# Kernel optimization log

Hardware: AMD Instinct MI355X
Metric: run time of the kernel (lower is better)

## Reference

```python
import jax, jax.numpy as jnp
import numpy as np

N = 8192
H = 512

def setup_inputs() -> dict:
    key = jax.random.key(0)
    ks = jax.random.split(key, 11)
    s = 1.0 / np.sqrt(H)
    return {
        "q": jax.random.normal(ks[0], (N, H), dtype=jnp.float32),
        "k": jax.random.normal(ks[1], (N, H), dtype=jnp.float32),
        "v": jax.random.normal(ks[2], (N, H), dtype=jnp.float32),
        "Wq": jax.random.uniform(ks[3], (H, H), jnp.float32, -s, s),
        "bq": jax.random.uniform(ks[4], (H,), jnp.float32, -s, s),
        "Wk": jax.random.uniform(ks[5], (H, H), jnp.float32, -s, s),
        "bk": jax.random.uniform(ks[6], (H,), jnp.float32, -s, s),
        "Wv": jax.random.uniform(ks[7], (H, H), jnp.float32, -s, s),
        "bv": jax.random.uniform(ks[8], (H,), jnp.float32, -s, s),
        "Wo": jax.random.uniform(ks[9], (H, H), jnp.float32, -s, s),
        "bo": jax.random.uniform(ks[10], (H,), jnp.float32, -s, s),
    }

def reference(q, k, v, Wq, bq, Wk, bk, Wv, bv, Wo, bo):
    # torch Linear: x @ W.T + b
    qp = q @ Wq.T + bq            # [N, H]
    kp = k @ Wk.T + bk            # [N, H]
    vp = v @ Wv.T + bv            # [N, H]
    weights = qp @ kp.T           # [N, N]  (no 1/sqrt(d) scaling in original)
    normalized = jax.nn.softmax(weights, axis=-1)  # [N, N]
    out = normalized @ vp         # [N, H]
    out = out @ Wo.T + bo         # [N, H]
    return (out, normalized)
```

## Files before the change

### kernel.cpp

```cpp
#include <hip/hip_runtime.h>

typedef unsigned short u16;
typedef _Float16 f16x8 __attribute__((ext_vector_type(8)));
typedef u16 u16x8 __attribute__((ext_vector_type(8)));
typedef float floatx4 __attribute__((ext_vector_type(4)));

#define DEV __device__ __forceinline__

DEV u16 f2h(float f) {
  _Float16 h = (_Float16)f;
  return __builtin_bit_cast(u16, h);
}

typedef __attribute__((address_space(3))) void lds_void_t;
typedef const __attribute__((address_space(1))) void gbl_void_t;

DEV void async16(const void* g, void* l) {
  __builtin_amdgcn_global_load_lds((gbl_void_t*)g, (lds_void_t*)l, 16, 0, 0);
}

template <int N>
DEV void wait_vm() {
  static_assert(N == 0 || N == 6 || N == 8 || N == 9 || N == 12,
                "add vmcnt literal");
  if constexpr (N == 0) asm volatile("s_waitcnt vmcnt(0)" ::: "memory");
  else if constexpr (N == 6) asm volatile("s_waitcnt vmcnt(6)" ::: "memory");
  else if constexpr (N == 8) asm volatile("s_waitcnt vmcnt(8)" ::: "memory");
  else if constexpr (N == 9) asm volatile("s_waitcnt vmcnt(9)" ::: "memory");
  else if constexpr (N == 12) asm volatile("s_waitcnt vmcnt(12)" ::: "memory");
}


__global__ __launch_bounds__(256) void k_cvt16(const float* __restrict__ x,
                                               u16* __restrict__ o, int n4) {
  int i = blockIdx.x * 256 + threadIdx.x;
  if (i >= n4) return;
  float4 v = ((const float4*)x)[i];
  *(ushort4*)&o[4 * (size_t)i] =
      make_ushort4(f2h(v.x), f2h(v.y), f2h(v.z), f2h(v.w));
}


__global__ __launch_bounds__(256) void k_transpose(const u16* __restrict__ in,
                                                   u16* __restrict__ out,
                                                   int R, int C) {
  __shared__ u16 T[64][72];
  int m0 = blockIdx.x * 64;
  int n0 = blockIdx.y * 64;
  int t = threadIdx.x;
#pragma unroll
  for (int i = 0; i < 2; ++i) {
    int lin = i * 2048 + t * 8;
    int r = lin >> 6, c = lin & 63;
    u16x8 d = *(const u16x8*)&in[(size_t)(m0 + r) * C + n0 + c];
#pragma unroll
    for (int j = 0; j < 8; ++j) T[r][c + j] = d[j];
  }
  __syncthreads();
#pragma unroll
  for (int i = 0; i < 2; ++i) {
    int lin = i * 2048 + t * 8;
    int r = lin >> 6, c = lin & 63;
    u16x8 d;
#pragma unroll
    for (int j = 0; j < 8; ++j) d[j] = T[c + j][r];
    *(u16x8*)&out[(size_t)(n0 + r) * R + m0 + c] = d;
  }
}


template <bool WRITEP>
__global__ __launch_bounds__(256) void k_softmax(float* __restrict__ W,
                                                 u16* __restrict__ P) {
  const size_t row = blockIdx.x;
  float4* pv = (float4*)(W + row * 8192);
  const int t = threadIdx.x;
  const int w = t >> 6, l = t & 63;
  float4 v[8];
#pragma unroll
  for (int i = 0; i < 8; ++i) v[i] = pv[i * 256 + t];
  float m = -1e30f;
#pragma unroll
  for (int i = 0; i < 8; ++i)
    m = fmaxf(m, fmaxf(fmaxf(v[i].x, v[i].y), fmaxf(v[i].z, v[i].w)));
#pragma unroll
  for (int o = 32; o >= 1; o >>= 1) m = fmaxf(m, __shfl_xor(m, o, 64));
  __shared__ float redm[4];
  __shared__ float reds[4];
  if (l == 0) redm[w] = m;
  __syncthreads();
  m = fmaxf(fmaxf(redm[0], redm[1]), fmaxf(redm[2], redm[3]));
  float s = 0.f;
#pragma unroll
  for (int i = 0; i < 8; ++i) {
    v[i].x = __expf(v[i].x - m); s += v[i].x;
    v[i].y = __expf(v[i].y - m); s += v[i].y;
    v[i].z = __expf(v[i].z - m); s += v[i].z;
    v[i].w = __expf(v[i].w - m); s += v[i].w;
  }
#pragma unroll
  for (int o = 32; o >= 1; o >>= 1) s += __shfl_xor(s, o, 64);
  if (l == 0) reds[w] = s;
  __syncthreads();
  s = (reds[0] + reds[1]) + (reds[2] + reds[3]);
  float inv = 1.0f / s;
#pragma unroll
  for (int i = 0; i < 8; ++i) {
    v[i].x *= inv; v[i].y *= inv; v[i].z *= inv; v[i].w *= inv;
    pv[i * 256 + t] = v[i];
    if constexpr (WRITEP) {
      *(ushort4*)&P[row * 8192 + (size_t)(i * 256 + t) * 4] =
          make_ushort4(f2h(v[i].x), f2h(v[i].y), f2h(v[i].z), f2h(v[i].w));
    }
  }
}


template <int BN, bool AF32, int OMODE, bool BIAS>
__global__ __launch_bounds__(256, 2)
void k_gemm(const void* A_, const u16* __restrict__ Bh,
            const float* __restrict__ bias, void* C_, int K, int lda, int ldb,
            int ldc) {
  constexpr int NT = BN / 32;
  constexpr int BCHW = BN / 64;
  constexpr int D = (BN == 128) ? 3 : 4;
  constexpr int BC = AF32 ? 1 : (D + 1);
  constexpr int LPI = 2 + BCHW;
  __shared__ alignas(16) u16 Ash[BC][128 * 32];
  __shared__ alignas(16) u16 Bsh[BC][BN * 32];

  const int m0 = blockIdx.x * 128;
  const int n0 = blockIdx.y * BN;
  const int tid = threadIdx.x;
  const int w = tid >> 6;
  const int l = tid & 63;
  const int lr = l & 15;
  const int lq = l >> 4;
  const int wr = (w >> 1) * 64;
  const int wc = (w & 1) * (BN / 2);
  const int srow = l >> 2;
  const int scolsw = ((l & 3) ^ ((l >> 3) & 3)) * 8;
  const int sw8 = (lq ^ ((lr >> 1) & 3)) * 8;

  const u16* Ah = (const u16*)A_;
  const float* Af = (const float*)A_;

  floatx4 acc[4][NT] = {};

  if constexpr (!AF32) {
    const int nIter = K / 32;
    auto STAGE = [&](int t, int b) {
      const int k0 = (t < nIter ? t : nIter - 1) * 32;
#pragma unroll
      for (int i = 0; i < 2; ++i) {
        int c = w * 2 + i;
        int row = c * 16 + srow;
        async16(Ah + (size_t)(m0 + row) * lda + k0 + scolsw, &Ash[b][c * 512]);
      }
#pragma unroll
      for (int i = 0; i < BCHW; ++i) {
        int c = w * BCHW + i;
        int row = c * 16 + srow;
        async16(Bh + (size_t)(n0 + row) * ldb + k0 + scolsw, &Bsh[b][c * 512]);
      }
    };

#pragma unroll
    for (int t = 0; t < D; ++t) STAGE(t, t);

    int bcon = 0;
    int bpro = D % BC;
    for (int t = 0; t < nIter; ++t) {
      wait_vm<LPI * (D - 1)>();
      __builtin_amdgcn_s_barrier();
      STAGE(t + D, bpro);

      f16x8 fa[4], fb[NT];
#pragma unroll
      for (int x = 0; x < 4; ++x)
        fa[x] = *(const f16x8*)&Ash[bcon][(wr + x * 16 + lr) * 32 + sw8];
#pragma unroll
      for (int x = 0; x < NT; ++x)
        fb[x] = *(const f16x8*)&Bsh[bcon][(wc + x * 16 + lr) * 32 + sw8];
#pragma unroll
      for (int mt = 0; mt < 4; ++mt)
#pragma unroll
        for (int nt = 0; nt < NT; ++nt)
          acc[mt][nt] = __builtin_amdgcn_mfma_f32_16x16x32_f16(
              fa[mt], fb[nt], acc[mt][nt], 0, 0, 0);

      if (++bcon == BC) bcon = 0;
      if (++bpro == BC) bpro = 0;
    }
  } else {
    for (int k0 = 0; k0 < K; k0 += 32) {
      __syncthreads();
#pragma unroll
      for (int i = 0; i < 2; ++i) {
        int lin = i * 2048 + tid * 8;
        int row = lin >> 5, col = lin & 31;
        const float* g = Af + (size_t)(m0 + row) * lda + k0 + col;
        float4 u0 = *(const float4*)g;
        float4 u1 = *(const float4*)(g + 4);
        u16x8 tv;
        tv[0] = f2h(u0.x); tv[1] = f2h(u0.y); tv[2] = f2h(u0.z); tv[3] = f2h(u0.w);
        tv[4] = f2h(u1.x); tv[5] = f2h(u1.y); tv[6] = f2h(u1.z); tv[7] = f2h(u1.w);
        int slot = (col >> 3) ^ ((row >> 1) & 3);
        *(u16x8*)&Ash[0][row * 32 + slot * 8] = tv;
      }
#pragma unroll
      for (int i = 0; i < BCHW; ++i) {
        int c = w * BCHW + i;
        int row = c * 16 + srow;
        async16(Bh + (size_t)(n0 + row) * ldb + k0 + scolsw, &Bsh[0][c * 512]);
      }
      __syncthreads();

      f16x8 fa[4], fb[NT];
#pragma unroll
      for (int x = 0; x < 4; ++x)
        fa[x] = *(const f16x8*)&Ash[0][(wr + x * 16 + lr) * 32 + sw8];
#pragma unroll
      for (int x = 0; x < NT; ++x)
        fb[x] = *(const f16x8*)&Bsh[0][(wc + x * 16 + lr) * 32 + sw8];
#pragma unroll
      for (int mt = 0; mt < 4; ++mt)
#pragma unroll
        for (int nt = 0; nt < NT; ++nt)
          acc[mt][nt] = __builtin_amdgcn_mfma_f32_16x16x32_f16(
              fa[mt], fb[nt], acc[mt][nt], 0, 0, 0);
    }
  }

  float bv[NT];
#pragma unroll
  for (int nt = 0; nt < NT; ++nt)
    bv[nt] = BIAS ? bias[n0 + wc + nt * 16 + lr] : 0.f;
#pragma unroll
  for (int mt = 0; mt < 4; ++mt)
#pragma unroll
    for (int nt = 0; nt < NT; ++nt)
#pragma unroll
      for (int r = 0; r < 4; ++r) {
        float x = acc[mt][nt][r] + bv[nt];
        int row = m0 + wr + mt * 16 + lq * 4 + r;
        int col = n0 + wc + nt * 16 + lr;
        size_t idx = (size_t)row * ldc + col;
        if constexpr (OMODE == 0) {
          ((float*)C_)[idx] = x;
        } else {
          ((u16*)C_)[idx] = f2h(x);
        }
      }
}


extern "C" void kernel_launch(void* const* d_in, const int* in_sizes, int n_in,
                              void* d_out, int out_size, void* d_ws,
                              size_t ws_size, hipStream_t stream) {
  constexpr int N = 8192, H = 512;
  const float* q   = (const float*)d_in[0];
  const float* kin = (const float*)d_in[1];
  const float* v   = (const float*)d_in[2];
  const float* Wq  = (const float*)d_in[3];
  const float* bq  = (const float*)d_in[4];
  const float* Wk  = (const float*)d_in[5];
  const float* bk  = (const float*)d_in[6];
  const float* Wv  = (const float*)d_in[7];
  const float* bv  = (const float*)d_in[8];
  const float* Wo  = (const float*)d_in[9];
  const float* bo  = (const float*)d_in[10];
  float* out  = (float*)d_out;
  float* norm = out + (size_t)N * H;

  char* ws = (char*)d_ws;
  const size_t MB = 1024 * 1024;
  u16* xh   = (u16*)(ws + 0 * MB);
  u16* wb   = (u16*)(ws + 8 * MB);
  u16* qp   = (u16*)(ws + 9 * MB);
  u16* kp   = (u16*)(ws + 17 * MB);
  u16* vp   = (u16*)(ws + 25 * MB);
  u16* vpT  = (u16*)(ws + 33 * MB);
  u16* Pf   = (u16*)(ws + 41 * MB);
  u16* out0 = vp;

  const bool usePf = ws_size >= 41 * MB + (size_t)N * N * 2;

  dim3 blk(256);

  k_cvt16<<<4096, blk, 0, stream>>>(q, xh, (N * H) / 4);
  k_cvt16<<<256, blk, 0, stream>>>(Wq, wb, (H * H) / 4);
  k_gemm<64, false, 1, true><<<dim3(64, 8), blk, 0, stream>>>(
      xh, wb, bq, qp, H, H, H, H);

  k_cvt16<<<4096, blk, 0, stream>>>(kin, xh, (N * H) / 4);
  k_cvt16<<<256, blk, 0, stream>>>(Wk, wb, (H * H) / 4);
  k_gemm<64, false, 1, true><<<dim3(64, 8), blk, 0, stream>>>(
      xh, wb, bk, kp, H, H, H, H);

  k_cvt16<<<4096, blk, 0, stream>>>(v, xh, (N * H) / 4);
  k_cvt16<<<256, blk, 0, stream>>>(Wv, wb, (H * H) / 4);
  k_gemm<64, false, 1, true><<<dim3(64, 8), blk, 0, stream>>>(
      xh, wb, bv, vp, H, H, H, H);
  k_transpose<<<dim3(128, 8), blk, 0, stream>>>(vp, vpT, N, H);

  k_gemm<128, false, 0, false><<<dim3(64, 64), blk, 0, stream>>>(
      qp, kp, nullptr, norm, H, H, H, N);

  if (usePf)
    k_softmax<true><<<N, blk, 0, stream>>>(norm, Pf);
  else
    k_softmax<false><<<N, blk, 0, stream>>>(norm, nullptr);

  if (usePf)
    k_gemm<64, false, 1, false><<<dim3(64, 8), blk, 0, stream>>>(
        Pf, vpT, nullptr, out0, N, N, N, H);
  else
    k_gemm<64, true, 1, false><<<dim3(64, 8), blk, 0, stream>>>(
        norm, vpT, nullptr, out0, N, N, N, H);

  k_cvt16<<<256, blk, 0, stream>>>(Wo, wb, (H * H) / 4);
  k_gemm<64, false, 0, true><<<dim3(64, 8), blk, 0, stream>>>(
      out0, wb, bo, out, H, H, H, H);
}
```

Baseline: 751.4 us.

## Split-K the P@V GemM into four slices with a reduction kernel

The P@V GEMM (K=8192) now runs as four K-slices across a z grid dimension, each writing fp32 partial sums to workspace, and a new reduction kernel adds them and converts to fp16. The goal is more blocks than the 512-block grid (64x8) so the GPU is filled during this long-K GEMM. Pipeline depth drops to 2 stages for all GEMMs, and launch-bounds occupancy hints become per-call (3 for QK^T, 4 for P@V), which cuts LDS use and raises occupancy. The cost is extra fp32 partial traffic plus one more launch, and the shallower prefetch could expose memory latency in the other GEMMs.

```diff
diff --git a/kernel.cpp b/kernel.cpp
--- a/kernel.cpp
+++ b/kernel.cpp
@@ -21,9 +21,12 @@
 
 template <int N>
 DEV void wait_vm() {
-  static_assert(N == 0 || N == 6 || N == 8 || N == 9 || N == 12,
+  static_assert(N == 0 || N == 3 || N == 4 || N == 6 || N == 8 || N == 9 ||
+                    N == 12,
                 "add vmcnt literal");
   if constexpr (N == 0) asm volatile("s_waitcnt vmcnt(0)" ::: "memory");
+  else if constexpr (N == 3) asm volatile("s_waitcnt vmcnt(3)" ::: "memory");
+  else if constexpr (N == 4) asm volatile("s_waitcnt vmcnt(4)" ::: "memory");
   else if constexpr (N == 6) asm volatile("s_waitcnt vmcnt(6)" ::: "memory");
   else if constexpr (N == 8) asm volatile("s_waitcnt vmcnt(8)" ::: "memory");
   else if constexpr (N == 9) asm volatile("s_waitcnt vmcnt(9)" ::: "memory");
@@ -38,6 +41,23 @@
   float4 v = ((const float4*)x)[i];
   *(ushort4*)&o[4 * (size_t)i] =
       make_ushort4(f2h(v.x), f2h(v.y), f2h(v.z), f2h(v.w));
+}
+
+
+__global__ __launch_bounds__(256) void k_red4(const float* __restrict__ p,
+                                              size_t pstride,
+                                              u16* __restrict__ o, int n4) {
+  int i = blockIdx.x * 256 + threadIdx.x;
+  if (i >= n4) return;
+  float4 a = ((const float4*)p)[i];
+  float4 b = ((const float4*)(p + pstride))[i];
+  float4 c = ((const float4*)(p + 2 * pstride))[i];
+  float4 d = ((const float4*)(p + 3 * pstride))[i];
+  *(ushort4*)&o[4 * (size_t)i] =
+      make_ushort4(f2h((a.x + b.x) + (c.x + d.x)),
+                   f2h((a.y + b.y) + (c.y + d.y)),
+                   f2h((a.z + b.z) + (c.z + d.z)),
+                   f2h((a.w + b.w) + (c.w + d.w)));
 }
 
 
@@ -116,14 +136,14 @@
 }
 
 
-template <int BN, bool AF32, int OMODE, bool BIAS>
-__global__ __launch_bounds__(256, 2)
+template <int BN, bool AF32, int OMODE, bool BIAS, int MINW>
+__global__ __launch_bounds__(256, MINW)
 void k_gemm(const void* A_, const u16* __restrict__ Bh,
             const float* __restrict__ bias, void* C_, int K, int lda, int ldb,
-            int ldc) {
+            int ldc, size_t zstride) {
   constexpr int NT = BN / 32;
   constexpr int BCHW = BN / 64;
-  constexpr int D = (BN == 128) ? 3 : 4;
+  constexpr int D = 2;
   constexpr int BC = AF32 ? 1 : (D + 1);
   constexpr int LPI = 2 + BCHW;
   __shared__ alignas(16) u16 Ash[BC][128 * 32];
@@ -131,6 +151,7 @@
 
   const int m0 = blockIdx.x * 128;
   const int n0 = blockIdx.y * BN;
+  const int kz = blockIdx.z * K;
   const int tid = threadIdx.x;
   const int w = tid >> 6;
   const int l = tid & 63;
@@ -150,7 +171,7 @@
   if constexpr (!AF32) {
     const int nIter = K / 32;
     auto STAGE = [&](int t, int b) {
-      const int k0 = (t < nIter ? t : nIter - 1) * 32;
+      const int k0 = kz + (t < nIter ? t : nIter - 1) * 32;
 #pragma unroll
       for (int i = 0; i < 2; ++i) {
         int c = w * 2 + i;
@@ -245,7 +266,7 @@
         float x = acc[mt][nt][r] + bv[nt];
         int row = m0 + wr + mt * 16 + lq * 4 + r;
         int col = n0 + wc + nt * 16 + lr;
-        size_t idx = (size_t)row * ldc + col;
+        size_t idx = (size_t)row * ldc + col + blockIdx.z * zstride;
         if constexpr (OMODE == 0) {
           ((float*)C_)[idx] = x;
         } else {
@@ -282,44 +303,51 @@
   u16* vp   = (u16*)(ws + 25 * MB);
   u16* vpT  = (u16*)(ws + 33 * MB);
   u16* Pf   = (u16*)(ws + 41 * MB);
+  float* pS = (float*)(ws + 169 * MB);
   u16* out0 = vp;
 
-  const bool usePf = ws_size >= 41 * MB + (size_t)N * N * 2;
+  const bool usePf    = ws_size >= 169 * MB;
+  const bool useSplit = ws_size >= 233 * MB;
 
   dim3 blk(256);
 
   k_cvt16<<<4096, blk, 0, stream>>>(q, xh, (N * H) / 4);
   k_cvt16<<<256, blk, 0, stream>>>(Wq, wb, (H * H) / 4);
-  k_gemm<64, false, 1, true><<<dim3(64, 8), blk, 0, stream>>>(
-      xh, wb, bq, qp, H, H, H, H);
+  k_gemm<64, false, 1, true, 2><<<dim3(64, 8), blk, 0, stream>>>(
+      xh, wb, bq, qp, H, H, H, H, 0);
 
   k_cvt16<<<4096, blk, 0, stream>>>(kin, xh, (N * H) / 4);
   k_cvt16<<<256, blk, 0, stream>>>(Wk, wb, (H * H) / 4);
-  k_gemm<64, false, 1, true><<<dim3(64, 8), blk, 0, stream>>>(
-      xh, wb, bk, kp, H, H, H, H);
+  k_gemm<64, false, 1, true, 2><<<dim3(64, 8), blk, 0, stream>>>(
+      xh, wb, bk, kp, H, H, H, H, 0);
 
   k_cvt16<<<4096, blk, 0, stream>>>(v, xh, (N * H) / 4);
   k_cvt16<<<256, blk, 0, stream>>>(Wv, wb, (H * H) / 4);
-  k_gemm<64, false, 1, true><<<dim3(64, 8), blk, 0, stream>>>(
-      xh, wb, bv, vp, H, H, H, H);
+  k_gemm<64, false, 1, true, 2><<<dim3(64, 8), blk, 0, stream>>>(
+      xh, wb, bv, vp, H, H, H, H, 0);
   k_transpose<<<dim3(128, 8), blk, 0, stream>>>(vp, vpT, N, H);
 
-  k_gemm<128, false, 0, false><<<dim3(64, 64), blk, 0, stream>>>(
-      qp, kp, nullptr, norm, H, H, H, N);
+  k_gemm<128, false, 0, false, 3><<<dim3(64, 64), blk, 0, stream>>>(
+      qp, kp, nullptr, norm, H, H, H, N, 0);
 
   if (usePf)
     k_softmax<true><<<N, blk, 0, stream>>>(norm, Pf);
   else
     k_softmax<false><<<N, blk, 0, stream>>>(norm, nullptr);
 
-  if (usePf)
-    k_gemm<64, false, 1, false><<<dim3(64, 8), blk, 0, stream>>>(
-        Pf, vpT, nullptr, out0, N, N, N, H);
-  else
-    k_gemm<64, true, 1, false><<<dim3(64, 8), blk, 0, stream>>>(
-        norm, vpT, nullptr, out0, N, N, N, H);
+  if (usePf && useSplit) {
+    k_gemm<64, false, 0, false, 4><<<dim3(64, 8, 4), blk, 0, stream>>>(
+        Pf, vpT, nullptr, pS, N / 4, N, N, H, (size_t)N * H);
+    k_red4<<<4096, blk, 0, stream>>>(pS, (size_t)N * H, out0, (N * H) / 4);
+  } else if (usePf) {
+    k_gemm<64, false, 1, false, 4><<<dim3(64, 8), blk, 0, stream>>>(
+        Pf, vpT, nullptr, out0, N, N, N, H, 0);
+  } else {
+    k_gemm<64, true, 1, false, 2><<<dim3(64, 8), blk, 0, stream>>>(
+        norm, vpT, nullptr, out0, N, N, N, H, 0);
+  }
 
   k_cvt16<<<256, blk, 0, stream>>>(Wo, wb, (H * H) / 4);
-  k_gemm<64, false, 0, true><<<dim3(64, 8), blk, 0, stream>>>(
-      out0, wb, bo, out, H, H, H, H);
-}
+  k_gemm<64, false, 0, true, 2><<<dim3(64, 8), blk, 0, stream>>>(
+      out0, wb, bo, out, H, H, H, H, 0);
+}
```

After: 719.9 us. -4.2%, faster.
